# Optimization experiments

Measured on AMD Instinct MI355X. Metric: run time of the kernel, lower is better.

## Reference

```python
import jax, jax.numpy as jnp
import numpy as np

EPS = 1e-5

def _ternary_ste(w):
    # STEQuantize: round(w/scale) clamped to [-1,1]; straight-through gradient.
    scale = jnp.maximum(jnp.mean(jnp.abs(w)), EPS)
    q = jnp.clip(jnp.round(w / scale), -1.0, 1.0)
    return w + jax.lax.stop_gradient(q - w)

def _bitlinear(x, w):
    # BitLinear: y = x @ (ternary(w) * scale)^T, scale = mean|w| (differentiable).
    scale = jnp.maximum(jnp.mean(jnp.abs(w)), EPS)
    return x @ (_ternary_ste(w) * scale).T

def _op_library(x, indices, weights, ops):
    # ops: (n_ops, D, D). Per-op ternary quantize + scale, then one batched einsum
    # instead of the python loop of small matmuls.
    n_ops = ops.shape[0]
    scales = jnp.maximum(jnp.mean(jnp.abs(ops), axis=(1, 2)), EPS)  # (n_ops,)
    q = jnp.clip(jnp.round(ops / scales[:, None, None]), -1.0, 1.0)
    w_eff = (ops + jax.lax.stop_gradient(q - ops)) * scales[:, None, None]  # (n,o,d)
    # transformed[n] = x @ w_eff[n]^T  ->  (B, S, n_ops, D)
    T = jnp.einsum('bsd,nod->bsno', x, w_eff)
    out = (1e-5 / n_ops) * jnp.sum(T, axis=2)
    gathered = jnp.take_along_axis(T, indices[:, :, :, None], axis=2)  # (B,S,K,D)
    out = out + jnp.sum(weights[..., None] * gathered, axis=2)
    return out

def _mem_read(x, slots, W_read):
    d = slots.shape[1]
    key = x @ W_read.T
    attn = jax.nn.softmax(key @ slots.T / jnp.sqrt(jnp.float32(d)), axis=-1)
    return attn @ slots

def _layernorm(x, gamma, beta):
    mu = jnp.mean(x, axis=-1, keepdims=True)
    var = jnp.var(x, axis=-1, keepdims=True)
    return (x - mu) * jax.lax.rsqrt(var + EPS) * gamma + beta

def _single_pass(reason, ops, W_router, slots, W_read, W_mix, ln_gamma, ln_beta, top_k):
    logits = _bitlinear(reason, W_router)              # (B,S,n_ops)
    vals, indices = jax.lax.top_k(logits, top_k)       # (B,S,K)
    weights = jax.nn.softmax(vals, axis=-1)
    op_out = _op_library(reason, indices, weights, ops)
    mem_out = _mem_read(reason, slots, W_read)
    mixed = jnp.concatenate([op_out, mem_out], axis=-1) @ W_mix.T
    return _layernorm(reason + mixed, ln_gamma, ln_beta)

def _write_signal(q, slots, W_wk, W_wg, W_wv):
    d = slots.shape[1]
    wk = q @ W_wk.T
    wg = jax.nn.sigmoid(q @ W_wg.T)                    # (B,S,1)
    wv = q @ W_wv.T
    addr = jax.nn.softmax(wk @ slots.T / jnp.sqrt(jnp.float32(d)), axis=-1)
    return wg * wv + 0.1 * (addr @ slots)

def setup_inputs() -> dict:
    key = jax.random.key(0)
    ks = jax.random.split(key, 12)
    B, S, d_model, d_reason = 8, 2048, 1024, 128
    n_ops, n_slots = 32, 16
    return {
        'hidden': jax.random.normal(ks[0], (B, S, d_model), jnp.float32),
        'force_depth': 2,
        'W_down': jax.random.normal(ks[1], (d_reason, d_model), jnp.float32) * 0.02,
        'W_up': jax.random.normal(ks[2], (d_model, d_reason), jnp.float32) * 0.02,
        'ops': jax.random.normal(ks[3], (n_ops, d_reason, d_reason), jnp.float32) * 0.02,
        'W_router': jax.random.normal(ks[4], (n_ops, d_reason), jnp.float32) * 0.02,
        'slots': jax.random.normal(ks[5], (n_slots, d_reason), jnp.float32) * 0.01,
        'W_read': jax.random.normal(ks[6], (d_reason, d_reason), jnp.float32) * 0.02,
        'W_wk': jax.random.normal(ks[7], (d_reason, d_reason), jnp.float32) * 0.02,
        'W_wg': jax.random.normal(ks[8], (1, d_reason), jnp.float32) * 0.02,
        'W_wv': jax.random.normal(ks[9], (d_reason, d_reason), jnp.float32) * 0.02,
        'W_mix': jax.random.normal(ks[10], (d_reason, 2 * d_reason), jnp.float32) * 0.02,
        'ln_gamma': jnp.ones((d_reason,), jnp.float32),
        'ln_beta': jnp.zeros((d_reason,), jnp.float32),
        'write_scale': jnp.float32(0.01),
    }

def reference(hidden, force_depth, W_down, W_up, ops, W_router, slots, W_read,
              W_wk, W_wg, W_wv, W_mix, ln_gamma, ln_beta, write_scale):
    top_k = 2
    reason = _bitlinear(hidden, W_down)
    for _ in range(int(force_depth)):
        reason = _single_pass(reason, ops, W_router, slots, W_read, W_mix,
                              ln_gamma, ln_beta, top_k)
    reason = reason + write_scale * _write_signal(reason, slots, W_wk, W_wg, W_wv)
    out = _bitlinear(reason, W_up)
    return hidden + out
```

## Files before the change

### kernel.cpp

```cpp
#include <hip/hip_runtime.h>


#define DR   128
#define DM   1024
#define NTOK 16384
#define NOPS 32
#define COEF (1e-5f / 32.f)

typedef __attribute__((ext_vector_type(8))) short bfrag;
typedef __attribute__((ext_vector_type(4))) float f32x4;

__device__ __forceinline__ ushort f2b_bits(float f) {
  union { float f; uint i; } c; c.f = f;
  uint x = c.i;
  return (ushort)((x + 0x7fffu + ((x >> 16) & 1u)) >> 16);
}
__device__ __forceinline__ float qeff(float w, float s) {
  float q = rintf(w / s);
  q = fminf(1.f, fmaxf(-1.f, q));
  return q * s;
}
__device__ __forceinline__ float waveRed(float v) {
#pragma unroll
  for (int m = 32; m > 0; m >>= 1) v += __shfl_xor(v, m, 64);
  return v;
}

#define OFF_SUMS    0
#define OFF_OPSSC   256
#define OFF_WDE     512
#define OFF_WUE     (OFF_WDE + 262144)
#define OFF_WRT     (OFF_WUE + 262144)
#define OFF_OPSB    (OFF_WRT + 16384)
#define OFF_WMIXA   (OFF_OPSB + 1048576)
#define OFF_WWVB    (OFF_WMIXA + 32768)
#define OFF_MRS     (OFF_WWVB + 32768)
#define OFF_MWS     (OFF_MRS + 8192)
#define OFF_SB      (OFF_MWS + 8192)
#define OFF_SLOTS   (OFF_SB + 8192)
#define OFF_WWG     (OFF_SLOTS + 8192)
#define OFF_GAMMA   (OFF_WWG + 512)
#define OFF_BETA    (OFF_GAMMA + 512)
#define OFF_WSC     (OFF_BETA + 512)
#define OFF_RF      (OFF_WSC + 256)
#define WS_TOTAL    (OFF_RF + 4194304)

__global__ __launch_bounds__(256) void k_absum_all(
    const float* __restrict__ W_down, const float* __restrict__ W_router,
    const float* __restrict__ W_up, const float* __restrict__ ops,
    float* __restrict__ sums) {
  __shared__ float ws4[4];
  const int y = blockIdx.y;
  const float* src; int n; float* dst;
  if (y == 0)      { src = W_down;   n = 131072; dst = &sums[0]; }
  else if (y == 1) { src = W_router; n = 4096;   dst = &sums[1]; }
  else if (y == 2) { src = W_up;     n = 131072; dst = &sums[2]; }
  else { src = ops + (size_t)(y - 3) * 16384; n = 16384; dst = &sums[y]; }
  float s = 0.f;
  for (int i = blockIdx.x * 256 + threadIdx.x; i < n; i += 8 * 256)
    s += fabsf(src[i]);
  s = waveRed(s);
  int lane = threadIdx.x & 63, wv = threadIdx.x >> 6;
  if (lane == 0) ws4[wv] = s;
  __syncthreads();
  if (threadIdx.x == 0) atomicAdd(dst, ws4[0] + ws4[1] + ws4[2] + ws4[3]);
}

__global__ __launch_bounds__(256) void k_build(
    const float* __restrict__ W_down, const float* __restrict__ W_up,
    const float* __restrict__ W_router, const float* __restrict__ ops,
    const float* __restrict__ W_read, const float* __restrict__ W_wk,
    const float* __restrict__ W_wg, const float* __restrict__ W_wv,
    const float* __restrict__ W_mix, const float* __restrict__ slots,
    const float* __restrict__ gamma, const float* __restrict__ beta,
    const float* __restrict__ wscale, int has_wsc, const float* __restrict__ sums,
    ushort* __restrict__ WdE, ushort* __restrict__ WuE, float* __restrict__ WrT,
    ushort* __restrict__ opsB, float* __restrict__ opsScale,
    ushort* __restrict__ WmixA, ushort* __restrict__ WwvB,
    float* __restrict__ Mrs, float* __restrict__ Mws, float* __restrict__ SBw,
    float* __restrict__ slotsF, float* __restrict__ WwgF,
    float* __restrict__ gammaF, float* __restrict__ betaF, float* __restrict__ wscF) {
  int id = blockIdx.x * 256 + threadIdx.x;
  const float s_wd = fmaxf(sums[0] * (1.f / 131072.f), 1e-5f);
  const float s_wr = fmaxf(sums[1] * (1.f / 4096.f), 1e-5f);
  const float s_wu = fmaxf(sums[2] * (1.f / 131072.f), 1e-5f);

  if (id < 131072) { WdE[id] = f2b_bits(qeff(W_down[id], s_wd)); return; }
  id -= 131072;
  if (id < 131072) { WuE[id] = f2b_bits(qeff(W_up[id], s_wu)); return; }
  id -= 131072;
  if (id < 4096) {
    int d = id >> 5, n = id & 31;
    WrT[id] = qeff(W_router[n * DR + d], s_wr);
    return;
  }
  id -= 4096;
  if (id < 524288) {
    int n = id >> 14;
    float s = fmaxf(sums[3 + n] * (1.f / 16384.f), 1e-5f);
    float q = rintf(ops[id] / s);
    q = fminf(1.f, fmaxf(-1.f, q));
    opsB[id] = f2b_bits(q);
    return;
  }
  id -= 524288;
  if (id < 32) { opsScale[id] = fmaxf(sums[3 + id] * (1.f / 16384.f), 1e-5f); return; }
  id -= 32;
  if (id < 16384) {
    int r = id >> 7, o = id & 127;
    WmixA[id] = f2b_bits(W_mix[r * 256 + o]);
    return;
  }
  id -= 16384;
  if (id < 16384) { WwvB[id] = f2b_bits(W_wv[id]); return; }
  id -= 16384;
  if (id < 2048) {
    int d = id >> 4, j = id & 15;
    float a = 0.f;
#pragma unroll 8
    for (int o = 0; o < DR; ++o) a += W_read[o * DR + d] * slots[j * DR + o];
    Mrs[id] = a;
    return;
  }
  id -= 2048;
  if (id < 2048) {
    int d = id >> 4, j = id & 15;
    float a = 0.f;
#pragma unroll 8
    for (int o = 0; o < DR; ++o) a += W_wk[o * DR + d] * slots[j * DR + o];
    Mws[id] = a;
    return;
  }
  id -= 2048;
  if (id < 2048) {
    int j = id >> 7, r = id & 127;
    float a = 0.f;
#pragma unroll 8
    for (int o = 0; o < DR; ++o) a += slots[j * DR + o] * W_mix[r * 256 + 128 + o];
    SBw[id] = a;
    return;
  }
  id -= 2048;
  if (id < 2048) { slotsF[id] = slots[id]; return; }
  id -= 2048;
  if (id < 128) { WwgF[id] = W_wg[id]; return; }
  id -= 128;
  if (id < 128) { gammaF[id] = gamma[id]; return; }
  id -= 128;
  if (id < 128) { betaF[id] = beta[id]; return; }
  id -= 128;
  if (id == 0) { wscF[0] = has_wsc ? wscale[0] : 0.01f; }
}

__global__ __launch_bounds__(256) void k_down(const float* __restrict__ hidden,
                                              const ushort* __restrict__ WdE,
                                              float* __restrict__ X) {
  const int w = threadIdx.x >> 6, lane = threadIdx.x & 63;
  const int quad = lane >> 4, mrow = lane & 15;
  const int m0 = blockIdx.x * 16;
  const int c0 = w * 32;

  f32x4 acc[2];
  acc[0] = (f32x4){0.f, 0.f, 0.f, 0.f};
  acc[1] = (f32x4){0.f, 0.f, 0.f, 0.f};

  const float* Ap = hidden + (size_t)(m0 + mrow) * DM + quad * 8;
#pragma unroll 2
  for (int kt = 0; kt < 32; ++kt) {
    float4 a0 = *(const float4*)(Ap + kt * 32);
    float4 a1 = *(const float4*)(Ap + kt * 32 + 4);
    bfrag a;
    a[0] = (short)f2b_bits(a0.x); a[1] = (short)f2b_bits(a0.y);
    a[2] = (short)f2b_bits(a0.z); a[3] = (short)f2b_bits(a0.w);
    a[4] = (short)f2b_bits(a1.x); a[5] = (short)f2b_bits(a1.y);
    a[6] = (short)f2b_bits(a1.z); a[7] = (short)f2b_bits(a1.w);
#pragma unroll
    for (int nt = 0; nt < 2; ++nt) {
      bfrag b = *(const bfrag*)(WdE + (size_t)(c0 + nt * 16 + mrow) * DM + kt * 32 + quad * 8);
      acc[nt] = __builtin_amdgcn_mfma_f32_16x16x32_bf16(a, b, acc[nt], 0, 0, 0);
    }
  }
#pragma unroll
  for (int nt = 0; nt < 2; ++nt)
#pragma unroll
    for (int r = 0; r < 4; ++r)
      X[(size_t)(m0 + quad * 4 + r) * DR + c0 + nt * 16 + mrow] = acc[nt][r];
}

__global__ __launch_bounds__(512) void k_pass2(
    float* __restrict__ X, ushort* __restrict__ RF, int emit,
    const float* __restrict__ WrT, const ushort* __restrict__ opsB,
    const float* __restrict__ opsScale, const ushort* __restrict__ WmixA,
    const float* __restrict__ Mrs, const float* __restrict__ SBw,
    const float* __restrict__ gammaF, const float* __restrict__ betaF,
    const ushort* __restrict__ WwvB, const float* __restrict__ Mws,
    const float* __restrict__ slotsF, const float* __restrict__ WwgF,
    const float* __restrict__ wscF) {
  __shared__ float  xsf[64][132];
  __shared__ ushort xsb[64][136];
  __shared__ float  lg[64][33];
  __shared__ float  coefT[32][64];
  __shared__ float  attn[64][17];
  __shared__ float  at2[64][17];
  __shared__ int    seli[64][2];
  __shared__ float  selw[64][2];
  __shared__ float  gp[64];
  __shared__ float  partS[8][4][4];
  __shared__ float  partQ[8][4][4];

  const int tid = threadIdx.x;
  const int w = tid >> 6, lane = tid & 63;
  const int quad = lane >> 4, mrow = lane & 15;
  const int t0 = blockIdx.x * 64;

  for (int i = tid; i < 2048; i += 512) {
    float4 v = *(const float4*)(X + (size_t)t0 * DR + i * 4);
    int t = i >> 5, c = (i & 31) * 4;
    xsf[t][c] = v.x; xsf[t][c + 1] = v.y; xsf[t][c + 2] = v.z; xsf[t][c + 3] = v.w;
    xsb[t][c] = f2b_bits(v.x); xsb[t][c + 1] = f2b_bits(v.y);
    xsb[t][c + 2] = f2b_bits(v.z); xsb[t][c + 3] = f2b_bits(v.w);
  }
  __syncthreads();

  for (int p = tid; p < 2048; p += 512) {
    int t = p >> 5, n = p & 31;
    const float4* xr = (const float4*)&xsf[t][0];
    float a = 0.f;
#pragma unroll 8
    for (int d4 = 0; d4 < 32; ++d4) {
      float4 x = xr[d4];
      a += x.x * WrT[(d4 * 4 + 0) * 32 + n];
      a += x.y * WrT[(d4 * 4 + 1) * 32 + n];
      a += x.z * WrT[(d4 * 4 + 2) * 32 + n];
      a += x.w * WrT[(d4 * 4 + 3) * 32 + n];
    }
    lg[t][n] = a;
  }
  for (int p = tid; p < 1024; p += 512) {
    int t = p >> 4, j = p & 15;
    const float4* xr = (const float4*)&xsf[t][0];
    float a = 0.f;
#pragma unroll 8
    for (int d4 = 0; d4 < 32; ++d4) {
      float4 x = xr[d4];
      a += x.x * Mrs[(d4 * 4 + 0) * 16 + j];
      a += x.y * Mrs[(d4 * 4 + 1) * 16 + j];
      a += x.z * Mrs[(d4 * 4 + 2) * 16 + j];
      a += x.w * Mrs[(d4 * 4 + 3) * 16 + j];
    }
    attn[t][j] = a * 0.088388347648318447f;
  }
  __syncthreads();

  if (tid < 64) {
    float v0 = -1e30f; int i0 = 0;
#pragma unroll
    for (int n = 0; n < 32; ++n) { float v = lg[tid][n]; if (v > v0) { v0 = v; i0 = n; } }
    float v1 = -1e30f; int i1 = 0;
#pragma unroll
    for (int n = 0; n < 32; ++n)
      if (n != i0) { float v = lg[tid][n]; if (v > v1) { v1 = v; i1 = n; } }
    float e = expf(v1 - v0);
    float w0 = 1.f / (1.f + e);
    seli[tid][0] = i0; seli[tid][1] = i1;
    selw[tid][0] = w0; selw[tid][1] = e * w0;
  } else if (tid < 128) {
    const int t = tid - 64;
    float m = -1e30f;
#pragma unroll
    for (int j = 0; j < 16; ++j) m = fmaxf(m, attn[t][j]);
    float s = 0.f;
#pragma unroll
    for (int j = 0; j < 16; ++j) { float ee = expf(attn[t][j] - m); attn[t][j] = ee; s += ee; }
    float inv = 1.f / s;
#pragma unroll
    for (int j = 0; j < 16; ++j) attn[t][j] *= inv;
  }
  __syncthreads();

  for (int p = tid; p < 2048; p += 512) {
    int n = p >> 6, t = p & 63;
    float cf = COEF;
    if (n == seli[t][0]) cf += selw[t][0];
    if (n == seli[t][1]) cf += selw[t][1];
    coefT[n][t] = cf * opsScale[n];
  }
  __syncthreads();

  bfrag a[4][4];
#pragma unroll
  for (int m = 0; m < 4; ++m)
#pragma unroll
    for (int kt = 0; kt < 4; ++kt)
      a[m][kt] = *(const bfrag*)&xsb[m * 16 + mrow][kt * 32 + quad * 8];

  const ushort* Bp = opsB + (size_t)(w * 16 + mrow) * DR + quad * 8;
  bfrag bc[4], bn[4];
#pragma unroll
  for (int kt = 0; kt < 4; ++kt) bc[kt] = *(const bfrag*)(Bp + kt * 32);

  f32x4 out[4];
#pragma unroll
  for (int m = 0; m < 4; ++m) out[m] = (f32x4){0.f, 0.f, 0.f, 0.f};

  for (int n = 0; n < NOPS; ++n) {
    if (n + 1 < NOPS) {
      const ushort* Bn = Bp + (size_t)(n + 1) * (DR * DR);
#pragma unroll
      for (int kt = 0; kt < 4; ++kt) bn[kt] = *(const bfrag*)(Bn + kt * 32);
    }
    f32x4 tmp[4];
#pragma unroll
    for (int m = 0; m < 4; ++m) tmp[m] = (f32x4){0.f, 0.f, 0.f, 0.f};
#pragma unroll
    for (int kt = 0; kt < 4; ++kt)
#pragma unroll
      for (int m = 0; m < 4; ++m)
        tmp[m] = __builtin_amdgcn_mfma_f32_16x16x32_bf16(a[m][kt], bc[kt], tmp[m], 0, 0, 0);
#pragma unroll
    for (int m = 0; m < 4; ++m) {
      f32x4 cf = *(const f32x4*)&coefT[n][m * 16 + quad * 4];
      out[m] += cf * tmp[m];
    }
    if (n + 1 < NOPS) {
#pragma unroll
      for (int kt = 0; kt < 4; ++kt) bc[kt] = bn[kt];
    }
  }
  __syncthreads();

#pragma unroll
  for (int m = 0; m < 4; ++m)
#pragma unroll
    for (int r = 0; r < 4; ++r)
      xsb[m * 16 + quad * 4 + r][w * 16 + mrow] = f2b_bits(out[m][r]);
  __syncthreads();

  const int mtile = w & 3;
  const int ch = (w >> 2) * 64;
  {
    bfrag a2[4];
#pragma unroll
    for (int kt = 0; kt < 4; ++kt)
      a2[kt] = *(const bfrag*)&xsb[mtile * 16 + mrow][kt * 32 + quad * 8];

    f32x4 acc[4];
#pragma unroll
    for (int i = 0; i < 4; ++i) acc[i] = (f32x4){0.f, 0.f, 0.f, 0.f};
#pragma unroll
    for (int kt = 0; kt < 4; ++kt)
#pragma unroll
      for (int nt = 0; nt < 4; ++nt) {
        bfrag b = *(const bfrag*)(WmixA + (size_t)(ch + nt * 16 + mrow) * DR + kt * 32 + quad * 8);
        acc[nt] = __builtin_amdgcn_mfma_f32_16x16x32_bf16(a2[kt], b, acc[nt], 0, 0, 0);
      }

    float v[4][4];
#pragma unroll
    for (int nt = 0; nt < 4; ++nt) {
      const int col = ch + nt * 16 + mrow;
#pragma unroll
      for (int r = 0; r < 4; ++r) {
        const int t = mtile * 16 + quad * 4 + r;
        float y0 = 0.f;
#pragma unroll
        for (int j = 0; j < 16; ++j) y0 += attn[t][j] * SBw[j * 128 + col];
        v[nt][r] = acc[nt][r] + xsf[t][col] + y0;
      }
    }
    float s[4], q[4];
#pragma unroll
    for (int r = 0; r < 4; ++r) {
      float ps = 0.f, pq = 0.f;
#pragma unroll
      for (int nt = 0; nt < 4; ++nt) { ps += v[nt][r]; pq += v[nt][r] * v[nt][r]; }
      s[r] = ps; q[r] = pq;
    }
#pragma unroll
    for (int m = 1; m < 16; m <<= 1)
#pragma unroll
      for (int r = 0; r < 4; ++r) {
        s[r] += __shfl_xor(s[r], m, 64);
        q[r] += __shfl_xor(q[r], m, 64);
      }
    if (mrow == 0)
#pragma unroll
      for (int r = 0; r < 4; ++r) { partS[w][quad][r] = s[r]; partQ[w][quad][r] = q[r]; }
    __syncthreads();

    float mu[4], rsd[4];
#pragma unroll
    for (int r = 0; r < 4; ++r) {
      float ts = s[r] + partS[w ^ 4][quad][r];
      float tq = q[r] + partQ[w ^ 4][quad][r];
      mu[r] = ts * (1.f / DR);
      float var = tq * (1.f / DR) - mu[r] * mu[r];
      rsd[r] = rsqrtf(var + 1e-5f);
    }
    if (!emit) {
#pragma unroll
      for (int nt = 0; nt < 4; ++nt) {
        const int col = ch + nt * 16 + mrow;
        const float g = gammaF[col], bb = betaF[col];
#pragma unroll
        for (int r = 0; r < 4; ++r) {
          const int t = mtile * 16 + quad * 4 + r;
          X[(size_t)(t0 + t) * DR + col] = (v[nt][r] - mu[r]) * rsd[r] * g + bb;
        }
      }
      return;
    }
#pragma unroll
    for (int nt = 0; nt < 4; ++nt) {
      const int col = ch + nt * 16 + mrow;
      const float g = gammaF[col], bb = betaF[col];
#pragma unroll
      for (int r = 0; r < 4; ++r) {
        const int t = mtile * 16 + quad * 4 + r;
        float val = (v[nt][r] - mu[r]) * rsd[r] * g + bb;
        xsf[t][col] = val;
        xsb[t][col] = f2b_bits(val);
      }
    }
  }
  __syncthreads();

  for (int p = tid; p < 1024; p += 512) {
    int t = p >> 4, j = p & 15;
    const float4* xr = (const float4*)&xsf[t][0];
    float a = 0.f;
#pragma unroll 8
    for (int d4 = 0; d4 < 32; ++d4) {
      float4 x = xr[d4];
      a += x.x * Mws[(d4 * 4 + 0) * 16 + j];
      a += x.y * Mws[(d4 * 4 + 1) * 16 + j];
      a += x.z * Mws[(d4 * 4 + 2) * 16 + j];
      a += x.w * Mws[(d4 * 4 + 3) * 16 + j];
    }
    at2[t][j] = a * 0.088388347648318447f;
  }
  __syncthreads();

  if (tid < 64) {
    const float4* xr = (const float4*)&xsf[tid][0];
    float z = 0.f;
#pragma unroll 8
    for (int d4 = 0; d4 < 32; ++d4) {
      float4 x = xr[d4];
      z += x.x * WwgF[d4 * 4 + 0] + x.y * WwgF[d4 * 4 + 1]
         + x.z * WwgF[d4 * 4 + 2] + x.w * WwgF[d4 * 4 + 3];
    }
    gp[tid] = wscF[0] / (1.f + expf(-z));
  } else if (tid < 128) {
    const int t = tid - 64;
    float m = -1e30f;
#pragma unroll
    for (int j = 0; j < 16; ++j) m = fmaxf(m, at2[t][j]);
    float s = 0.f;
#pragma unroll
    for (int j = 0; j < 16; ++j) { float e = expf(at2[t][j] - m); at2[t][j] = e; s += e; }
    float inv = 1.f / s;
#pragma unroll
    for (int j = 0; j < 16; ++j) at2[t][j] *= inv;
  }
  __syncthreads();

  {
    bfrag a2[4];
#pragma unroll
    for (int kt = 0; kt < 4; ++kt)
      a2[kt] = *(const bfrag*)&xsb[mtile * 16 + mrow][kt * 32 + quad * 8];

    f32x4 acc[4];
#pragma unroll
    for (int i = 0; i < 4; ++i) acc[i] = (f32x4){0.f, 0.f, 0.f, 0.f};
#pragma unroll
    for (int kt = 0; kt < 4; ++kt)
#pragma unroll
      for (int nt = 0; nt < 4; ++nt) {
        bfrag b = *(const bfrag*)(WwvB + (size_t)(ch + nt * 16 + mrow) * DR + kt * 32 + quad * 8);
        acc[nt] = __builtin_amdgcn_mfma_f32_16x16x32_bf16(a2[kt], b, acc[nt], 0, 0, 0);
      }

    const float c01 = wscF[0] * 0.1f;
#pragma unroll
    for (int nt = 0; nt < 4; ++nt) {
      const int col = ch + nt * 16 + mrow;
#pragma unroll
      for (int r = 0; r < 4; ++r) {
        const int t = mtile * 16 + quad * 4 + r;
        float mo = 0.f;
#pragma unroll
        for (int j = 0; j < 16; ++j) mo += at2[t][j] * slotsF[j * DR + col];
        float val = xsf[t][col] + gp[t] * acc[nt][r] + c01 * mo;
        RF[(size_t)(t0 + t) * DR + col] = f2b_bits(val);
      }
    }
  }
}

__global__ __launch_bounds__(256) void k_up(const ushort* __restrict__ Rf,
                                            const ushort* __restrict__ WuE,
                                            const float* __restrict__ hidden,
                                            float* __restrict__ out) {
  __shared__ float cs[64][132];

  const int wave = threadIdx.x >> 6, lane = threadIdx.x & 63;
  const int quad = lane >> 4, mrow = lane & 15;
  const int mt = blockIdx.x >> 3, ngrp = blockIdx.x & 7;
  const int m0b = mt * 64;
  const int m0 = m0b + wave * 16;
  const int c0 = ngrp * 128;

  f32x4 acc[8];
#pragma unroll
  for (int i = 0; i < 8; ++i) acc[i] = (f32x4){0.f, 0.f, 0.f, 0.f};

  const ushort* Ap = Rf + (size_t)(m0 + mrow) * DR + quad * 8;
#pragma unroll
  for (int kt = 0; kt < 4; ++kt) {
    bfrag a = *(const bfrag*)(Ap + kt * 32);
#pragma unroll
    for (int nt = 0; nt < 8; ++nt) {
      const ushort* Bp = WuE + (size_t)(c0 + nt * 16 + mrow) * DR + kt * 32 + quad * 8;
      bfrag b = *(const bfrag*)Bp;
      acc[nt] = __builtin_amdgcn_mfma_f32_16x16x32_bf16(a, b, acc[nt], 0, 0, 0);
    }
  }
#pragma unroll
  for (int nt = 0; nt < 8; ++nt)
#pragma unroll
    for (int r = 0; r < 4; ++r)
      cs[wave * 16 + quad * 4 + r][nt * 16 + mrow] = acc[nt][r];
  __syncthreads();

#pragma unroll
  for (int k = 0; k < 8; ++k) {
    const int i = threadIdx.x + k * 256;
    const int t = i >> 5, c4 = (i & 31) * 4;
    const size_t idx = (size_t)(m0b + t) * DM + c0 + c4;
    float4 h = *(const float4*)(hidden + idx);
    float4 v;
    v.x = h.x + cs[t][c4];
    v.y = h.y + cs[t][c4 + 1];
    v.z = h.z + cs[t][c4 + 2];
    v.w = h.w + cs[t][c4 + 3];
    *(float4*)(out + idx) = v;
  }
}

extern "C" void kernel_launch(void* const* d_in, const int* in_sizes, int n_in,
                              void* d_out, int out_size, void* d_ws, size_t ws_size,
                              hipStream_t stream) {
  int ns[20]; int nn = 0; int lastsc = -1;
  for (int i = 0; i < n_in; ++i) {
    if (in_sizes[i] == 1) lastsc = i;
    else if (nn < 20) ns[nn++] = i;
  }
  int iH = 0, iWd = 2, iWu = 3, iOps = 4, iWr = 5, iSl = 6, iRe = 7,
      iWk = 8, iWg = 9, iWv = 10, iMx = 11, iG = 12, iB = 13;
  if (nn >= 13) {
    iH  = ns[0];  iWd = ns[1];  iWu = ns[2];  iOps = ns[3]; iWr = ns[4];
    iSl = ns[5];  iRe = ns[6];  iWk = ns[7];  iWg = ns[8];  iWv = ns[9];
    iMx = ns[10]; iG  = ns[11]; iB  = ns[12];
  }
  const float* hidden   = (const float*)d_in[iH];
  const float* W_down   = (const float*)d_in[iWd];
  const float* W_up     = (const float*)d_in[iWu];
  const float* opsw     = (const float*)d_in[iOps];
  const float* W_router = (const float*)d_in[iWr];
  const float* slots    = (const float*)d_in[iSl];
  const float* W_read   = (const float*)d_in[iRe];
  const float* W_wk     = (const float*)d_in[iWk];
  const float* W_wg     = (const float*)d_in[iWg];
  const float* W_wv     = (const float*)d_in[iWv];
  const float* W_mix    = (const float*)d_in[iMx];
  const float* lng      = (const float*)d_in[iG];
  const float* lnb      = (const float*)d_in[iB];
  const float* wscale   = (lastsc >= 0) ? (const float*)d_in[lastsc] : (const float*)d_in[iG];
  const int has_wsc     = (lastsc >= 0) ? 1 : 0;

  char* ws = (char*)d_ws;
  float*  sums   = (float*)(ws + OFF_SUMS);
  float*  opsSc  = (float*)(ws + OFF_OPSSC);
  ushort* WdE    = (ushort*)(ws + OFF_WDE);
  ushort* WuE    = (ushort*)(ws + OFF_WUE);
  float*  WrT    = (float*)(ws + OFF_WRT);
  ushort* opsB   = (ushort*)(ws + OFF_OPSB);
  ushort* WmixA  = (ushort*)(ws + OFF_WMIXA);
  ushort* WwvB   = (ushort*)(ws + OFF_WWVB);
  float*  Mrs    = (float*)(ws + OFF_MRS);
  float*  Mws    = (float*)(ws + OFF_MWS);
  float*  SBw    = (float*)(ws + OFF_SB);
  float*  slotsF = (float*)(ws + OFF_SLOTS);
  float*  WwgF   = (float*)(ws + OFF_WWG);
  float*  gammaF = (float*)(ws + OFF_GAMMA);
  float*  betaF  = (float*)(ws + OFF_BETA);
  float*  wscF   = (float*)(ws + OFF_WSC);
  ushort* RF     = (ushort*)(ws + OFF_RF);

  float* X = (float*)d_out;

  hipMemsetAsync(ws + OFF_SUMS, 0, 256, stream);
  k_absum_all<<<dim3(8, 35), 256, 0, stream>>>(W_down, W_router, W_up, opsw, sums);
  k_build<<<3250, 256, 0, stream>>>(W_down, W_up, W_router, opsw, W_read, W_wk, W_wg,
                                    W_wv, W_mix, slots, lng, lnb, wscale, has_wsc,
                                    sums, WdE, WuE, WrT, opsB, opsSc, WmixA, WwvB,
                                    Mrs, Mws, SBw, slotsF, WwgF, gammaF, betaF, wscF);
  k_down<<<1024, 256, 0, stream>>>(hidden, WdE, X);
  k_pass2<<<256, 512, 0, stream>>>(X, RF, 0, WrT, opsB, opsSc, WmixA, Mrs, SBw,
                                   gammaF, betaF, WwvB, Mws, slotsF, WwgF, wscF);
  k_pass2<<<256, 512, 0, stream>>>(X, RF, 1, WrT, opsB, opsSc, WmixA, Mrs, SBw,
                                   gammaF, betaF, WwvB, Mws, slotsF, WwgF, wscF);
  k_up<<<2048, 256, 0, stream>>>(RF, WuE, hidden, X);
}
```

Before: 374.1 us.

## Fuse both reasoning passes into one kernel and drop memset in abs-sum reduction

The two launches of the per-pass kernel are merged into a single kernel that loops over both passes, keeping the 64-token tile in shared memory between them. This removes a full write and re-read of the intermediate reasoning state to global memory, plus one launch. Separately, the abs-sum reduction now uses one 1024-thread block per tensor with float4 loads and writes its result directly, which removes the memset and the atomics. The single-block reduction has less parallelism for the larger weight tensors.

```diff
diff --git a/kernel.cpp b/kernel.cpp
--- a/kernel.cpp
+++ b/kernel.cpp
@@ -45,25 +45,33 @@
 #define OFF_RF      (OFF_WSC + 256)
 #define WS_TOTAL    (OFF_RF + 4194304)
 
-__global__ __launch_bounds__(256) void k_absum_all(
+__global__ __launch_bounds__(1024) void k_absum_all(
     const float* __restrict__ W_down, const float* __restrict__ W_router,
     const float* __restrict__ W_up, const float* __restrict__ ops,
     float* __restrict__ sums) {
-  __shared__ float ws4[4];
-  const int y = blockIdx.y;
-  const float* src; int n; float* dst;
-  if (y == 0)      { src = W_down;   n = 131072; dst = &sums[0]; }
-  else if (y == 1) { src = W_router; n = 4096;   dst = &sums[1]; }
-  else if (y == 2) { src = W_up;     n = 131072; dst = &sums[2]; }
-  else { src = ops + (size_t)(y - 3) * 16384; n = 16384; dst = &sums[y]; }
+  __shared__ float ws16[16];
+  const int y = blockIdx.x;
+  const int tid = threadIdx.x;
+  const float* src; int n;
+  if (y == 0)      { src = W_down;   n = 131072; }
+  else if (y == 1) { src = W_router; n = 4096;   }
+  else if (y == 2) { src = W_up;     n = 131072; }
+  else             { src = ops + (size_t)(y - 3) * 16384; n = 16384; }
   float s = 0.f;
-  for (int i = blockIdx.x * 256 + threadIdx.x; i < n; i += 8 * 256)
-    s += fabsf(src[i]);
+  for (int i = tid * 4; i < n; i += 4096) {
+    float4 v = *(const float4*)(src + i);
+    s += fabsf(v.x) + fabsf(v.y) + fabsf(v.z) + fabsf(v.w);
+  }
   s = waveRed(s);
-  int lane = threadIdx.x & 63, wv = threadIdx.x >> 6;
-  if (lane == 0) ws4[wv] = s;
+  const int lane = tid & 63, wv = tid >> 6;
+  if (lane == 0) ws16[wv] = s;
   __syncthreads();
-  if (threadIdx.x == 0) atomicAdd(dst, ws4[0] + ws4[1] + ws4[2] + ws4[3]);
+  if (tid == 0) {
+    float t = 0.f;
+#pragma unroll
+    for (int i = 0; i < 16; ++i) t += ws16[i];
+    sums[y] = t;
+  }
 }
 
 __global__ __launch_bounds__(256) void k_build(
@@ -187,8 +195,8 @@
       X[(size_t)(m0 + quad * 4 + r) * DR + c0 + nt * 16 + mrow] = acc[nt][r];
 }
 
-__global__ __launch_bounds__(512) void k_pass2(
-    float* __restrict__ X, ushort* __restrict__ RF, int emit,
+__global__ __launch_bounds__(512) void k_passes(
+    const float* __restrict__ X, ushort* __restrict__ RF,
     const float* __restrict__ WrT, const ushort* __restrict__ opsB,
     const float* __restrict__ opsScale, const ushort* __restrict__ WmixA,
     const float* __restrict__ Mrs, const float* __restrict__ SBw,
@@ -222,182 +230,183 @@
   }
   __syncthreads();
 
-  for (int p = tid; p < 2048; p += 512) {
-    int t = p >> 5, n = p & 31;
-    const float4* xr = (const float4*)&xsf[t][0];
-    float a = 0.f;
+#pragma unroll 1
+  for (int pass = 0; pass < 2; ++pass) {
+    for (int p = tid; p < 2048; p += 512) {
+      int t = p >> 5, n = p & 31;
+      const float4* xr = (const float4*)&xsf[t][0];
+      float a = 0.f;
 #pragma unroll 8
-    for (int d4 = 0; d4 < 32; ++d4) {
-      float4 x = xr[d4];
-      a += x.x * WrT[(d4 * 4 + 0) * 32 + n];
-      a += x.y * WrT[(d4 * 4 + 1) * 32 + n];
-      a += x.z * WrT[(d4 * 4 + 2) * 32 + n];
-      a += x.w * WrT[(d4 * 4 + 3) * 32 + n];
-    }
-    lg[t][n] = a;
-  }
-  for (int p = tid; p < 1024; p += 512) {
-    int t = p >> 4, j = p & 15;
-    const float4* xr = (const float4*)&xsf[t][0];
-    float a = 0.f;
+      for (int d4 = 0; d4 < 32; ++d4) {
+        float4 x = xr[d4];
+        a += x.x * WrT[(d4 * 4 + 0) * 32 + n];
+        a += x.y * WrT[(d4 * 4 + 1) * 32 + n];
+        a += x.z * WrT[(d4 * 4 + 2) * 32 + n];
+        a += x.w * WrT[(d4 * 4 + 3) * 32 + n];
+      }
+      lg[t][n] = a;
+    }
+    for (int p = tid; p < 1024; p += 512) {
+      int t = p >> 4, j = p & 15;
+      const float4* xr = (const float4*)&xsf[t][0];
+      float a = 0.f;
 #pragma unroll 8
-    for (int d4 = 0; d4 < 32; ++d4) {
-      float4 x = xr[d4];
-      a += x.x * Mrs[(d4 * 4 + 0) * 16 + j];
-      a += x.y * Mrs[(d4 * 4 + 1) * 16 + j];
-      a += x.z * Mrs[(d4 * 4 + 2) * 16 + j];
-      a += x.w * Mrs[(d4 * 4 + 3) * 16 + j];
-    }
-    attn[t][j] = a * 0.088388347648318447f;
-  }
-  __syncthreads();
-
-  if (tid < 64) {
-    float v0 = -1e30f; int i0 = 0;
-#pragma unroll
-    for (int n = 0; n < 32; ++n) { float v = lg[tid][n]; if (v > v0) { v0 = v; i0 = n; } }
-    float v1 = -1e30f; int i1 = 0;
-#pragma unroll
-    for (int n = 0; n < 32; ++n)
-      if (n != i0) { float v = lg[tid][n]; if (v > v1) { v1 = v; i1 = n; } }
-    float e = expf(v1 - v0);
-    float w0 = 1.f / (1.f + e);
-    seli[tid][0] = i0; seli[tid][1] = i1;
-    selw[tid][0] = w0; selw[tid][1] = e * w0;
-  } else if (tid < 128) {
-    const int t = tid - 64;
-    float m = -1e30f;
-#pragma unroll
-    for (int j = 0; j < 16; ++j) m = fmaxf(m, attn[t][j]);
-    float s = 0.f;
-#pragma unroll
-    for (int j = 0; j < 16; ++j) { float ee = expf(attn[t][j] - m); attn[t][j] = ee; s += ee; }
-    float inv = 1.f / s;
-#pragma unroll
-    for (int j = 0; j < 16; ++j) attn[t][j] *= inv;
-  }
-  __syncthreads();
-
-  for (int p = tid; p < 2048; p += 512) {
-    int n = p >> 6, t = p & 63;
-    float cf = COEF;
-    if (n == seli[t][0]) cf += selw[t][0];
-    if (n == seli[t][1]) cf += selw[t][1];
-    coefT[n][t] = cf * opsScale[n];
-  }
-  __syncthreads();
-
-  bfrag a[4][4];
-#pragma unroll
-  for (int m = 0; m < 4; ++m)
-#pragma unroll
-    for (int kt = 0; kt < 4; ++kt)
-      a[m][kt] = *(const bfrag*)&xsb[m * 16 + mrow][kt * 32 + quad * 8];
-
-  const ushort* Bp = opsB + (size_t)(w * 16 + mrow) * DR + quad * 8;
-  bfrag bc[4], bn[4];
-#pragma unroll
-  for (int kt = 0; kt < 4; ++kt) bc[kt] = *(const bfrag*)(Bp + kt * 32);
-
-  f32x4 out[4];
-#pragma unroll
-  for (int m = 0; m < 4; ++m) out[m] = (f32x4){0.f, 0.f, 0.f, 0.f};
-
-  for (int n = 0; n < NOPS; ++n) {
-    if (n + 1 < NOPS) {
-      const ushort* Bn = Bp + (size_t)(n + 1) * (DR * DR);
-#pragma unroll
-      for (int kt = 0; kt < 4; ++kt) bn[kt] = *(const bfrag*)(Bn + kt * 32);
-    }
-    f32x4 tmp[4];
-#pragma unroll
-    for (int m = 0; m < 4; ++m) tmp[m] = (f32x4){0.f, 0.f, 0.f, 0.f};
-#pragma unroll
-    for (int kt = 0; kt < 4; ++kt)
-#pragma unroll
-      for (int m = 0; m < 4; ++m)
-        tmp[m] = __builtin_amdgcn_mfma_f32_16x16x32_bf16(a[m][kt], bc[kt], tmp[m], 0, 0, 0);
-#pragma unroll
-    for (int m = 0; m < 4; ++m) {
-      f32x4 cf = *(const f32x4*)&coefT[n][m * 16 + quad * 4];
-      out[m] += cf * tmp[m];
-    }
-    if (n + 1 < NOPS) {
-#pragma unroll
-      for (int kt = 0; kt < 4; ++kt) bc[kt] = bn[kt];
-    }
-  }
-  __syncthreads();
-
-#pragma unroll
-  for (int m = 0; m < 4; ++m)
-#pragma unroll
-    for (int r = 0; r < 4; ++r)
-      xsb[m * 16 + quad * 4 + r][w * 16 + mrow] = f2b_bits(out[m][r]);
-  __syncthreads();
-
-  const int mtile = w & 3;
-  const int ch = (w >> 2) * 64;
-  {
-    bfrag a2[4];
-#pragma unroll
-    for (int kt = 0; kt < 4; ++kt)
-      a2[kt] = *(const bfrag*)&xsb[mtile * 16 + mrow][kt * 32 + quad * 8];
-
-    f32x4 acc[4];
-#pragma unroll
-    for (int i = 0; i < 4; ++i) acc[i] = (f32x4){0.f, 0.f, 0.f, 0.f};
-#pragma unroll
-    for (int kt = 0; kt < 4; ++kt)
+      for (int d4 = 0; d4 < 32; ++d4) {
+        float4 x = xr[d4];
+        a += x.x * Mrs[(d4 * 4 + 0) * 16 + j];
+        a += x.y * Mrs[(d4 * 4 + 1) * 16 + j];
+        a += x.z * Mrs[(d4 * 4 + 2) * 16 + j];
+        a += x.w * Mrs[(d4 * 4 + 3) * 16 + j];
+      }
+      attn[t][j] = a * 0.088388347648318447f;
+    }
+    __syncthreads();
+
+    if (tid < 64) {
+      float v0 = -1e30f; int i0 = 0;
+#pragma unroll
+      for (int n = 0; n < 32; ++n) { float v = lg[tid][n]; if (v > v0) { v0 = v; i0 = n; } }
+      float v1 = -1e30f; int i1 = 0;
+#pragma unroll
+      for (int n = 0; n < 32; ++n)
+        if (n != i0) { float v = lg[tid][n]; if (v > v1) { v1 = v; i1 = n; } }
+      float e = expf(v1 - v0);
+      float w0 = 1.f / (1.f + e);
+      seli[tid][0] = i0; seli[tid][1] = i1;
+      selw[tid][0] = w0; selw[tid][1] = e * w0;
+    } else if (tid < 128) {
+      const int t = tid - 64;
+      float m = -1e30f;
+#pragma unroll
+      for (int j = 0; j < 16; ++j) m = fmaxf(m, attn[t][j]);
+      float s = 0.f;
+#pragma unroll
+      for (int j = 0; j < 16; ++j) { float ee = expf(attn[t][j] - m); attn[t][j] = ee; s += ee; }
+      float inv = 1.f / s;
+#pragma unroll
+      for (int j = 0; j < 16; ++j) attn[t][j] *= inv;
+    }
+    __syncthreads();
+
+    for (int p = tid; p < 2048; p += 512) {
+      int n = p >> 6, t = p & 63;
+      float cf = COEF;
+      if (n == seli[t][0]) cf += selw[t][0];
+      if (n == seli[t][1]) cf += selw[t][1];
+      coefT[n][t] = cf * opsScale[n];
+    }
+    __syncthreads();
+
+    bfrag a[4][4];
+#pragma unroll
+    for (int m = 0; m < 4; ++m)
+#pragma unroll
+      for (int kt = 0; kt < 4; ++kt)
+        a[m][kt] = *(const bfrag*)&xsb[m * 16 + mrow][kt * 32 + quad * 8];
+
+    const ushort* Bp = opsB + (size_t)(w * 16 + mrow) * DR + quad * 8;
+    bfrag bc[4], bn[4];
+#pragma unroll
+    for (int kt = 0; kt < 4; ++kt) bc[kt] = *(const bfrag*)(Bp + kt * 32);
+
+    f32x4 out[4];
+#pragma unroll
+    for (int m = 0; m < 4; ++m) out[m] = (f32x4){0.f, 0.f, 0.f, 0.f};
+
+    for (int n = 0; n < NOPS; ++n) {
+      if (n + 1 < NOPS) {
+        const ushort* Bn = Bp + (size_t)(n + 1) * (DR * DR);
+#pragma unroll
+        for (int kt = 0; kt < 4; ++kt) bn[kt] = *(const bfrag*)(Bn + kt * 32);
+      }
+      f32x4 tmp[4];
+#pragma unroll
+      for (int m = 0; m < 4; ++m) tmp[m] = (f32x4){0.f, 0.f, 0.f, 0.f};
+#pragma unroll
+      for (int kt = 0; kt < 4; ++kt)
+#pragma unroll
+        for (int m = 0; m < 4; ++m)
+          tmp[m] = __builtin_amdgcn_mfma_f32_16x16x32_bf16(a[m][kt], bc[kt], tmp[m], 0, 0, 0);
+#pragma unroll
+      for (int m = 0; m < 4; ++m) {
+        f32x4 cf = *(const f32x4*)&coefT[n][m * 16 + quad * 4];
+        out[m] += cf * tmp[m];
+      }
+      if (n + 1 < NOPS) {
+#pragma unroll
+        for (int kt = 0; kt < 4; ++kt) bc[kt] = bn[kt];
+      }
+    }
+    __syncthreads();
+
+#pragma unroll
+    for (int m = 0; m < 4; ++m)
+#pragma unroll
+      for (int r = 0; r < 4; ++r)
+        xsb[m * 16 + quad * 4 + r][w * 16 + mrow] = f2b_bits(out[m][r]);
+    __syncthreads();
+
+    const int mtile = w & 3;
+    const int ch = (w >> 2) * 64;
+    {
+      bfrag a2[4];
+#pragma unroll
+      for (int kt = 0; kt < 4; ++kt)
+        a2[kt] = *(const bfrag*)&xsb[mtile * 16 + mrow][kt * 32 + quad * 8];
+
+      f32x4 acc[4];
+#pragma unroll
+      for (int i = 0; i < 4; ++i) acc[i] = (f32x4){0.f, 0.f, 0.f, 0.f};
+#pragma unroll
+      for (int kt = 0; kt < 4; ++kt)
+#pragma unroll
+        for (int nt = 0; nt < 4; ++nt) {
+          bfrag b = *(const bfrag*)(WmixA + (size_t)(ch + nt * 16 + mrow) * DR + kt * 32 + quad * 8);
+          acc[nt] = __builtin_amdgcn_mfma_f32_16x16x32_bf16(a2[kt], b, acc[nt], 0, 0, 0);
+        }
+
+      float v[4][4];
 #pragma unroll
       for (int nt = 0; nt < 4; ++nt) {
-        bfrag b = *(const bfrag*)(WmixA + (size_t)(ch + nt * 16 + mrow) * DR + kt * 32 + quad * 8);
-        acc[nt] = __builtin_amdgcn_mfma_f32_16x16x32_bf16(a2[kt], b, acc[nt], 0, 0, 0);
-      }
-
-    float v[4][4];
-#pragma unroll
-    for (int nt = 0; nt < 4; ++nt) {
-      const int col = ch + nt * 16 + mrow;
+        const int col = ch + nt * 16 + mrow;
+#pragma unroll
+        for (int r = 0; r < 4; ++r) {
+          const int t = mtile * 16 + quad * 4 + r;
+          float y0 = 0.f;
+#pragma unroll
+          for (int j = 0; j < 16; ++j) y0 += attn[t][j] * SBw[j * 128 + col];
+          v[nt][r] = acc[nt][r] + xsf[t][col] + y0;
+        }
+      }
+      float s[4], q[4];
 #pragma unroll
       for (int r = 0; r < 4; ++r) {
-        const int t = mtile * 16 + quad * 4 + r;
-        float y0 = 0.f;
-#pragma unroll
-        for (int j = 0; j < 16; ++j) y0 += attn[t][j] * SBw[j * 128 + col];
-        v[nt][r] = acc[nt][r] + xsf[t][col] + y0;
-      }
-    }
-    float s[4], q[4];
-#pragma unroll
-    for (int r = 0; r < 4; ++r) {
-      float ps = 0.f, pq = 0.f;
-#pragma unroll
-      for (int nt = 0; nt < 4; ++nt) { ps += v[nt][r]; pq += v[nt][r] * v[nt][r]; }
-      s[r] = ps; q[r] = pq;
-    }
-#pragma unroll
-    for (int m = 1; m < 16; m <<= 1)
+        float ps = 0.f, pq = 0.f;
+#pragma unroll
+        for (int nt = 0; nt < 4; ++nt) { ps += v[nt][r]; pq += v[nt][r] * v[nt][r]; }
+        s[r] = ps; q[r] = pq;
+      }
+#pragma unroll
+      for (int m = 1; m < 16; m <<= 1)
+#pragma unroll
+        for (int r = 0; r < 4; ++r) {
+          s[r] += __shfl_xor(s[r], m, 64);
+          q[r] += __shfl_xor(q[r], m, 64);
+        }
+      if (mrow == 0)
+#pragma unroll
+        for (int r = 0; r < 4; ++r) { partS[w][quad][r] = s[r]; partQ[w][quad][r] = q[r]; }
+      __syncthreads();
+
+      float mu[4], rsd[4];
 #pragma unroll
       for (int r = 0; r < 4; ++r) {
-        s[r] += __shfl_xor(s[r], m, 64);
-        q[r] += __shfl_xor(q[r], m, 64);
-      }
-    if (mrow == 0)
-#pragma unroll
-      for (int r = 0; r < 4; ++r) { partS[w][quad][r] = s[r]; partQ[w][quad][r] = q[r]; }
-    __syncthreads();
-
-    float mu[4], rsd[4];
-#pragma unroll
-    for (int r = 0; r < 4; ++r) {
-      float ts = s[r] + partS[w ^ 4][quad][r];
-      float tq = q[r] + partQ[w ^ 4][quad][r];
-      mu[r] = ts * (1.f / DR);
-      float var = tq * (1.f / DR) - mu[r] * mu[r];
-      rsd[r] = rsqrtf(var + 1e-5f);
-    }
-    if (!emit) {
+        float ts = s[r] + partS[w ^ 4][quad][r];
+        float tq = q[r] + partQ[w ^ 4][quad][r];
+        mu[r] = ts * (1.f / DR);
+        float var = tq * (1.f / DR) - mu[r] * mu[r];
+        rsd[r] = rsqrtf(var + 1e-5f);
+      }
 #pragma unroll
       for (int nt = 0; nt < 4; ++nt) {
         const int col = ch + nt * 16 + mrow;
@@ -405,25 +414,14 @@
 #pragma unroll
         for (int r = 0; r < 4; ++r) {
           const int t = mtile * 16 + quad * 4 + r;
-          X[(size_t)(t0 + t) * DR + col] = (v[nt][r] - mu[r]) * rsd[r] * g + bb;
+          float val = (v[nt][r] - mu[r]) * rsd[r] * g + bb;
+          xsf[t][col] = val;
+          xsb[t][col] = f2b_bits(val);
         }
       }
-      return;
-    }
-#pragma unroll
-    for (int nt = 0; nt < 4; ++nt) {
-      const int col = ch + nt * 16 + mrow;
-      const float g = gammaF[col], bb = betaF[col];
-#pragma unroll
-      for (int r = 0; r < 4; ++r) {
-        const int t = mtile * 16 + quad * 4 + r;
-        float val = (v[nt][r] - mu[r]) * rsd[r] * g + bb;
-        xsf[t][col] = val;
-        xsb[t][col] = f2b_bits(val);
-      }
-    }
-  }
-  __syncthreads();
+    }
+    __syncthreads();
+  }
 
   for (int p = tid; p < 1024; p += 512) {
     int t = p >> 4, j = p & 15;
@@ -466,6 +464,8 @@
   __syncthreads();
 
   {
+    const int mtile = w & 3;
+    const int ch = (w >> 2) * 64;
     bfrag a2[4];
 #pragma unroll
     for (int kt = 0; kt < 4; ++kt)
@@ -601,16 +601,13 @@
 
   float* X = (float*)d_out;
 
-  hipMemsetAsync(ws + OFF_SUMS, 0, 256, stream);
-  k_absum_all<<<dim3(8, 35), 256, 0, stream>>>(W_down, W_router, W_up, opsw, sums);
+  k_absum_all<<<35, 1024, 0, stream>>>(W_down, W_router, W_up, opsw, sums);
   k_build<<<3250, 256, 0, stream>>>(W_down, W_up, W_router, opsw, W_read, W_wk, W_wg,
                                     W_wv, W_mix, slots, lng, lnb, wscale, has_wsc,
                                     sums, WdE, WuE, WrT, opsB, opsSc, WmixA, WwvB,
                                     Mrs, Mws, SBw, slotsF, WwgF, gammaF, betaF, wscF);
   k_down<<<1024, 256, 0, stream>>>(hidden, WdE, X);
-  k_pass2<<<256, 512, 0, stream>>>(X, RF, 0, WrT, opsB, opsSc, WmixA, Mrs, SBw,
-                                   gammaF, betaF, WwvB, Mws, slotsF, WwgF, wscF);
-  k_pass2<<<256, 512, 0, stream>>>(X, RF, 1, WrT, opsB, opsSc, WmixA, Mrs, SBw,
-                                   gammaF, betaF, WwvB, Mws, slotsF, WwgF, wscF);
+  k_passes<<<256, 512, 0, stream>>>(X, RF, WrT, opsB, opsSc, WmixA, Mrs, SBw,
+                                    gammaF, betaF, WwvB, Mws, slotsF, WwgF, wscF);
   k_up<<<2048, 256, 0, stream>>>(RF, WuE, hidden, X);
 }
```

Result: slower. 656.1 us (+75.4%).
